# Performance work log

Hardware: AMD Instinct MI355X
Metric: run time of the kernel (lower is better)

## Reference

```python
import jax, jax.numpy as jnp
import numpy as np
from jax import lax

K = 16
SIGMA2 = 1.0  # sigma=1.0 squared
EPS = 1e-06


def setup_inputs() -> dict:
    key = jax.random.key(0)
    xyz = jax.random.normal(key, (4, 3, 4096), dtype=jnp.float32)
    return {"xyz": xyz}


def reference(xyz):
    # xyz: (B, 3, N)
    B, _, N = xyz.shape
    pts = jnp.transpose(xyz, (0, 2, 1))  # (B, N, 3)

    sq = jnp.sum(pts * pts, axis=-1)  # (B, N)
    d2 = sq[:, :, None] + sq[:, None, :] - 2.0 * jnp.einsum("bnd,bmd->bnm", pts, pts)

    # k nearest neighbors (smallest distance, includes self like torch knn on same set)
    _, idx = lax.top_k(-d2, K)  # idx: (B, N, K)

    # gather neighbor coordinates and recompute exact squared distance (faithful to source)
    neighbors = jax.vmap(lambda p, i: p[i])(pts, idx)  # (B, N, K, 3)
    diff = pts[:, :, None, :] - neighbors
    dist2 = jnp.sum(diff * diff, axis=-1)  # (B, N, K)
    weights = jnp.exp(-dist2 / (2.0 * SIGMA2))

    # scatter k-sparse weights into dense adjacency (topk indices per row are unique)
    bb = jnp.arange(B)[:, None, None]
    ii = jnp.arange(N)[None, :, None]
    A = jnp.zeros((B, N, N), dtype=xyz.dtype).at[bb, ii, idx].set(weights)
    A = 0.5 * (A + jnp.swapaxes(A, 1, 2))

    # symmetric normalized Laplacian L = I - D^{-1/2} A D^{-1/2} (diag scaling via broadcast)
    D = jnp.clip(jnp.sum(A, axis=-1), EPS, None)
    d_is = D ** -0.5  # (B, N)
    L = jnp.eye(N, dtype=xyz.dtype)[None] - d_is[:, :, None] * A * d_is[:, None, :]
    return L
```

## Files before the change

### kernel.cpp

```cpp
#include <hip/hip_runtime.h>
#include <math.h>

#pragma clang fp contract(off)

#define NPTS 4096
#define KNN  16
#define RPW  2
#define KWAVES 8
#define KT   (KWAVES * 64)
#define RPBK (KWAVES * RPW)
#define CAP  128

__device__ __forceinline__ unsigned okey(float f) {
    f = f + 0.0f;
    unsigned u = __float_as_uint(f);
    return u ^ (((unsigned)((int)u >> 31)) | 0x80000000u);
}

__device__ __forceinline__ unsigned wmin32(unsigned v) {
    for (int o = 32; o > 0; o >>= 1) { unsigned w = __shfl_xor(v, o); v = w < v ? w : v; }
    return v;
}
__device__ __forceinline__ unsigned long long wmin64(unsigned long long v) {
    for (int o = 32; o > 0; o >>= 1) { unsigned long long w = __shfl_xor(v, o); v = w < v ? w : v; }
    return v;
}

__global__ __launch_bounds__(256) void fill_kernel(float4* __restrict__ L4,
                                                   float4* __restrict__ Dsum4,
                                                   size_t T4) {
    size_t g4     = (size_t)blockIdx.x * blockDim.x + threadIdx.x;
    size_t stride = (size_t)gridDim.x * blockDim.x;
    if (g4 < 4096) Dsum4[g4] = make_float4(0.f, 0.f, 0.f, 0.f);
    for (; g4 < T4; g4 += stride) {
        size_t g = g4 << 2;
        int o    = (int)(g & (size_t)(NPTS * (size_t)NPTS - 1));
        int row  = o >> 12;
        int col0 = o & (NPTS - 1);
        float4 v;
        v.x = (row == col0    ) ? 1.0f : 0.0f;
        v.y = (row == col0 + 1) ? 1.0f : 0.0f;
        v.z = (row == col0 + 2) ? 1.0f : 0.0f;
        v.w = (row == col0 + 3) ? 1.0f : 0.0f;
        L4[g4] = v;
    }
}

__global__ __launch_bounds__(KT, 4) void knn_kernel(const float* __restrict__ xyz,
                                                    float* __restrict__ Dsum,
                                                    int* __restrict__ idx_out,
                                                    float* __restrict__ w_out) {
    __shared__ float4 spts[NPTS];
    __shared__ int    lists[RPBK][CAP];

    const int t    = threadIdx.x;
    const int lane = t & 63;
    const int wv   = t >> 6;
    const int row0 = blockIdx.x * RPBK + wv * RPW;
    const int b    = row0 >> 12;
    const float* X = xyz + (size_t)b * 3 * NPTS;

    for (int i = t; i < NPTS; i += KT) {
        float x = X[i], y = X[NPTS + i], z = X[2 * NPTS + i];
        spts[i] = make_float4(x, y, z, (x * x + y * y) + z * z);
    }
    __syncthreads();

    const float4 P0 = spts[(row0 + 0) & (NPTS - 1)];
    const float4 P1 = spts[(row0 + 1) & (NPTS - 1)];

    unsigned b0 = 0xFFFFFFFFu, b1 = 0xFFFFFFFFu;
    for (int i = 0; i < NPTS / 64; ++i) {
        float4 Q   = spts[i * 64 + lane];
        float dot0 = (P0.x * Q.x + P0.y * Q.y) + P0.z * Q.z;
        float dot1 = (P1.x * Q.x + P1.y * Q.y) + P1.z * Q.z;
        unsigned k0 = okey((P0.w + Q.w) - 2.0f * dot0);
        unsigned k1 = okey((P1.w + Q.w) - 2.0f * dot1);
        b0 = k0 < b0 ? k0 : b0;
        b1 = k1 < b1 ? k1 : b1;
    }
    unsigned T0 = 0, T1 = 0;
    {
        unsigned cur = b0;
        for (int r = 0; r < KNN; ++r) { unsigned mn = wmin32(cur); T0 = mn; if (cur == mn) cur = 0xFFFFFFFFu; }
        cur = b1;
        for (int r = 0; r < KNN; ++r) { unsigned mn = wmin32(cur); T1 = mn; if (cur == mn) cur = 0xFFFFFFFFu; }
    }

    int cnt0 = 0, cnt1 = 0;
    for (int i = 0; i < NPTS / 64; ++i) {
        int m = i * 64 + lane;
        float4 Q   = spts[m];
        float dot0 = (P0.x * Q.x + P0.y * Q.y) + P0.z * Q.z;
        float dot1 = (P1.x * Q.x + P1.y * Q.y) + P1.z * Q.z;
        bool p0 = okey((P0.w + Q.w) - 2.0f * dot0) <= T0;
        bool p1 = okey((P1.w + Q.w) - 2.0f * dot1) <= T1;
        unsigned long long bal0 = __ballot(p0);
        unsigned long long bal1 = __ballot(p1);
        if (p0) {
            int pos = cnt0 + __popcll(bal0 & ((1ull << lane) - 1ull));
            if (pos < CAP) lists[wv * RPW + 0][pos] = m;
        }
        if (p1) {
            int pos = cnt1 + __popcll(bal1 & ((1ull << lane) - 1ull));
            if (pos < CAP) lists[wv * RPW + 1][pos] = m;
        }
        cnt0 += (int)__popcll(bal0);
        cnt1 += (int)__popcll(bal1);
    }

    for (int r = 0; r < RPW; ++r) {
        const int rowg = row0 + r;
        const float4 P = r == 0 ? P0 : P1;
        const int cnt  = r == 0 ? cnt0 : cnt1;
        const int lr   = wv * RPW + r;

        unsigned long long sel = ~0ull;
        if (cnt <= CAP) {
            unsigned long long e0 = ~0ull, e1 = ~0ull;
            if (lane < cnt) {
                int m = lists[lr][lane]; float4 Q = spts[m];
                float dot = (P.x * Q.x + P.y * Q.y) + P.z * Q.z;
                float d2  = (P.w + Q.w) - 2.0f * dot;
                e0 = ((unsigned long long)okey(d2) << 32) | (unsigned)m;
            }
            if (lane + 64 < cnt) {
                int m = lists[lr][lane + 64]; float4 Q = spts[m];
                float dot = (P.x * Q.x + P.y * Q.y) + P.z * Q.z;
                float d2  = (P.w + Q.w) - 2.0f * dot;
                e1 = ((unsigned long long)okey(d2) << 32) | (unsigned)m;
            }
            unsigned long long c = e0 < e1 ? e0 : e1;
            for (int k = 0; k < KNN; ++k) {
                unsigned long long mn = wmin64(c);
                if (c == mn) {
                    if (e0 == mn) e0 = ~0ull; else e1 = ~0ull;
                    c = e0 < e1 ? e0 : e1;
                }
                if (lane == k) sel = mn;
            }
        } else {
            unsigned long long last = 0;
            for (int k = 0; k < KNN; ++k) {
                unsigned long long bestp = ~0ull;
                for (int i = 0; i < NPTS / 64; ++i) {
                    int m = i * 64 + lane;
                    float4 Q  = spts[m];
                    float dot = (P.x * Q.x + P.y * Q.y) + P.z * Q.z;
                    float d2  = (P.w + Q.w) - 2.0f * dot;
                    unsigned long long key = ((unsigned long long)okey(d2) << 32) | (unsigned)m;
                    if (key > last && key < bestp) bestp = key;
                }
                unsigned long long mn = wmin64(bestp);
                if (lane == k) sel = mn;
                last = mn;
            }
        }

        float wgt = 0.0f;
        if (lane < KNN) {
            int j = (int)(unsigned)(sel & 0xFFFFFFFFull);
            float4 Q = spts[j];
            float dx = P.x - Q.x, dy = P.y - Q.y, dz = P.z - Q.z;
            float dist2 = (dx * dx + dy * dy) + dz * dz;
            wgt = expf(-(dist2 * 0.5f));
            size_t base = (size_t)rowg * KNN + lane;
            idx_out[base] = j;
            w_out[base]   = wgt;
            atomicAdd(&Dsum[(b << 12) + j], 0.5f * wgt);
        }
        float rs = wgt;
        for (int o = 32; o > 0; o >>= 1) rs += __shfl_xor(rs, o);
        if (lane == 0) atomicAdd(&Dsum[rowg], 0.5f * rs);
    }
}

__global__ __launch_bounds__(256) void scatter_kernel(const int* __restrict__ idxb,
                                                      const float* __restrict__ wb,
                                                      const float* __restrict__ Dsum,
                                                      float* __restrict__ L) {
    int g   = blockIdx.x * 256 + threadIdx.x;
    int row = g >> 4;
    int b   = row >> 12;
    int n   = row & (NPTS - 1);
    int j   = idxb[g];
    float sn = 1.0f / sqrtf(fmaxf(Dsum[row], 1e-6f));
    float sj = 1.0f / sqrtf(fmaxf(Dsum[(b << 12) + j], 1e-6f));
    float v  = -0.5f * wb[g] * sn * sj;
    float* Lb = L + (size_t)b * NPTS * NPTS;
    atomicAdd(Lb + (size_t)n * NPTS + j, v);
    atomicAdd(Lb + (size_t)j * NPTS + n, v);
}

extern "C" void kernel_launch(void* const* d_in, const int* in_sizes, int n_in,
                              void* d_out, int out_size, void* d_ws, size_t ws_size,
                              hipStream_t stream) {
    const float* xyz = (const float*)d_in[0];
    const int B  = in_sizes[0] / (3 * NPTS);
    const int BN = B * NPTS;

    float* Dsum = (float*)d_ws;
    int*   idxb = (int*)(Dsum + BN);
    float* wb   = (float*)(idxb + (size_t)BN * KNN);
    float* L    = (float*)d_out;

    size_t T4 = (size_t)B * NPTS * NPTS / 4;
    fill_kernel<<<8192, 256, 0, stream>>>((float4*)d_out, (float4*)Dsum, T4);
    knn_kernel<<<BN / RPBK, KT, 0, stream>>>(xyz, Dsum, idxb, wb);
    scatter_kernel<<<(BN * KNN) / 256, 256, 0, stream>>>(idxb, wb, Dsum, L);
}
```

Measured before the change: 371.2 us.

## Build per-row sparse adjacency lists and write each Laplacian row once

The old path filled the dense identity into L with a separate pass, then scattered each kNN edge into L with global atomics in both directions. Now the knn kernel appends every edge to per-row lists (capped at 96 entries) for both endpoints. A new row kernel accumulates each row in shared memory and writes the full dense L row once. This removes a full read-modify-write pass over the 256MB output and the scattered global atomics. It risks silently dropping edges if a point has more than 96 incoming neighbours, and the list order depends on atomic ordering.

```diff
diff --git a/kernel.cpp b/kernel.cpp
--- a/kernel.cpp
+++ b/kernel.cpp
@@ -10,6 +10,7 @@
 #define KT   (KWAVES * 64)
 #define RPBK (KWAVES * RPW)
 #define CAP  128
+#define CAP2 96
 
 __device__ __forceinline__ unsigned okey(float f) {
     f = f + 0.0f;
@@ -26,30 +27,16 @@
     return v;
 }
 
-__global__ __launch_bounds__(256) void fill_kernel(float4* __restrict__ L4,
-                                                   float4* __restrict__ Dsum4,
-                                                   size_t T4) {
-    size_t g4     = (size_t)blockIdx.x * blockDim.x + threadIdx.x;
-    size_t stride = (size_t)gridDim.x * blockDim.x;
-    if (g4 < 4096) Dsum4[g4] = make_float4(0.f, 0.f, 0.f, 0.f);
-    for (; g4 < T4; g4 += stride) {
-        size_t g = g4 << 2;
-        int o    = (int)(g & (size_t)(NPTS * (size_t)NPTS - 1));
-        int row  = o >> 12;
-        int col0 = o & (NPTS - 1);
-        float4 v;
-        v.x = (row == col0    ) ? 1.0f : 0.0f;
-        v.y = (row == col0 + 1) ? 1.0f : 0.0f;
-        v.z = (row == col0 + 2) ? 1.0f : 0.0f;
-        v.w = (row == col0 + 3) ? 1.0f : 0.0f;
-        L4[g4] = v;
-    }
+__global__ void zero_kernel(float* __restrict__ Dsum, int* __restrict__ cnt, int n) {
+    int i = blockIdx.x * blockDim.x + threadIdx.x;
+    if (i < n) { Dsum[i] = 0.0f; cnt[i] = 0; }
 }
 
 __global__ __launch_bounds__(KT, 4) void knn_kernel(const float* __restrict__ xyz,
                                                     float* __restrict__ Dsum,
-                                                    int* __restrict__ idx_out,
-                                                    float* __restrict__ w_out) {
+                                                    int* __restrict__ cnt,
+                                                    int* __restrict__ cols,
+                                                    float* __restrict__ vals) {
     __shared__ float4 spts[NPTS];
     __shared__ int    lists[RPBK][CAP];
 
@@ -111,20 +98,21 @@
 
     for (int r = 0; r < RPW; ++r) {
         const int rowg = row0 + r;
+        const int nloc = rowg & (NPTS - 1);
         const float4 P = r == 0 ? P0 : P1;
-        const int cnt  = r == 0 ? cnt0 : cnt1;
+        const int cn   = r == 0 ? cnt0 : cnt1;
         const int lr   = wv * RPW + r;
 
         unsigned long long sel = ~0ull;
-        if (cnt <= CAP) {
+        if (cn <= CAP) {
             unsigned long long e0 = ~0ull, e1 = ~0ull;
-            if (lane < cnt) {
+            if (lane < cn) {
                 int m = lists[lr][lane]; float4 Q = spts[m];
                 float dot = (P.x * Q.x + P.y * Q.y) + P.z * Q.z;
                 float d2  = (P.w + Q.w) - 2.0f * dot;
                 e0 = ((unsigned long long)okey(d2) << 32) | (unsigned)m;
             }
-            if (lane + 64 < cnt) {
+            if (lane + 64 < cn) {
                 int m = lists[lr][lane + 64]; float4 Q = spts[m];
                 float dot = (P.x * Q.x + P.y * Q.y) + P.z * Q.z;
                 float d2  = (P.w + Q.w) - 2.0f * dot;
@@ -164,10 +152,13 @@
             float dx = P.x - Q.x, dy = P.y - Q.y, dz = P.z - Q.z;
             float dist2 = (dx * dx + dy * dy) + dz * dz;
             wgt = expf(-(dist2 * 0.5f));
-            size_t base = (size_t)rowg * KNN + lane;
-            idx_out[base] = j;
-            w_out[base]   = wgt;
-            atomicAdd(&Dsum[(b << 12) + j], 0.5f * wgt);
+            float hw = 0.5f * wgt;
+            int jg = (b << 12) + j;
+            atomicAdd(&Dsum[jg], hw);
+            int p0 = atomicAdd(&cnt[rowg], 1);
+            if (p0 < CAP2) { cols[(size_t)rowg * CAP2 + p0] = j;    vals[(size_t)rowg * CAP2 + p0] = hw; }
+            int p1 = atomicAdd(&cnt[jg], 1);
+            if (p1 < CAP2) { cols[(size_t)jg * CAP2 + p1] = nloc;   vals[(size_t)jg * CAP2 + p1] = hw; }
         }
         float rs = wgt;
         for (int o = 32; o > 0; o >>= 1) rs += __shfl_xor(rs, o);
@@ -175,21 +166,42 @@
     }
 }
 
-__global__ __launch_bounds__(256) void scatter_kernel(const int* __restrict__ idxb,
-                                                      const float* __restrict__ wb,
-                                                      const float* __restrict__ Dsum,
-                                                      float* __restrict__ L) {
-    int g   = blockIdx.x * 256 + threadIdx.x;
-    int row = g >> 4;
-    int b   = row >> 12;
-    int n   = row & (NPTS - 1);
-    int j   = idxb[g];
-    float sn = 1.0f / sqrtf(fmaxf(Dsum[row], 1e-6f));
-    float sj = 1.0f / sqrtf(fmaxf(Dsum[(b << 12) + j], 1e-6f));
-    float v  = -0.5f * wb[g] * sn * sj;
-    float* Lb = L + (size_t)b * NPTS * NPTS;
-    atomicAdd(Lb + (size_t)n * NPTS + j, v);
-    atomicAdd(Lb + (size_t)j * NPTS + n, v);
+__global__ __launch_bounds__(256) void rowwrite_kernel(const int* __restrict__ cnt,
+                                                       const int* __restrict__ cols,
+                                                       const float* __restrict__ vals,
+                                                       const float* __restrict__ Dsum,
+                                                       float* __restrict__ L) {
+    __shared__ float acc[NPTS];
+    const int t  = threadIdx.x;
+    const int r  = blockIdx.x;
+    const int b  = r >> 12;
+    const int rl = r & (NPTS - 1);
+
+    for (int i = t; i < NPTS; i += 256) acc[i] = 0.0f;
+    __syncthreads();
+
+    int c_ = cnt[r]; if (c_ > CAP2) c_ = CAP2;
+    float sn = 1.0f / sqrtf(fmaxf(Dsum[r], 1e-6f));
+    for (int e = t; e < c_; e += 256) {
+        int   c = cols[(size_t)r * CAP2 + e];
+        float v = vals[(size_t)r * CAP2 + e];
+        float sc = 1.0f / sqrtf(fmaxf(Dsum[(b << 12) + c], 1e-6f));
+        atomicAdd(&acc[c], v * sn * sc);
+    }
+    __syncthreads();
+
+    float4* out4 = (float4*)(L + (size_t)b * NPTS * NPTS + (size_t)rl * NPTS);
+    const float4* a4 = (const float4*)acc;
+    for (int i4 = t; i4 < NPTS / 4; i4 += 256) {
+        float4 a = a4[i4];
+        int c0 = i4 << 2;
+        float4 v;
+        v.x = ((c0 + 0) == rl ? 1.0f : 0.0f) - a.x;
+        v.y = ((c0 + 1) == rl ? 1.0f : 0.0f) - a.y;
+        v.z = ((c0 + 2) == rl ? 1.0f : 0.0f) - a.z;
+        v.w = ((c0 + 3) == rl ? 1.0f : 0.0f) - a.w;
+        out4[i4] = v;
+    }
 }
 
 extern "C" void kernel_launch(void* const* d_in, const int* in_sizes, int n_in,
@@ -200,12 +212,12 @@
     const int BN = B * NPTS;
 
     float* Dsum = (float*)d_ws;
-    int*   idxb = (int*)(Dsum + BN);
-    float* wb   = (float*)(idxb + (size_t)BN * KNN);
+    int*   cnt  = (int*)(Dsum + BN);
+    int*   cols = cnt + BN;
+    float* vals = (float*)(cols + (size_t)BN * CAP2);
     float* L    = (float*)d_out;
 
-    size_t T4 = (size_t)B * NPTS * NPTS / 4;
-    fill_kernel<<<8192, 256, 0, stream>>>((float4*)d_out, (float4*)Dsum, T4);
-    knn_kernel<<<BN / RPBK, KT, 0, stream>>>(xyz, Dsum, idxb, wb);
-    scatter_kernel<<<(BN * KNN) / 256, 256, 0, stream>>>(idxb, wb, Dsum, L);
-}
+    zero_kernel<<<BN / 256, 256, 0, stream>>>(Dsum, cnt, BN);
+    knn_kernel<<<BN / RPBK, KT, 0, stream>>>(xyz, Dsum, cnt, cols, vals);
+    rowwrite_kernel<<<BN, 256, 0, stream>>>(cnt, cols, vals, Dsum, L);
+}
```

Measured after the change: 371.8 us. Within noise of the previous version (+0.2%).
